# Optimization experiments

Measured on AMD Instinct MI355X. Metric: run time of the kernel, lower is better.

The kernel has to match this reference:

```python
import jax, jax.numpy as jnp
import numpy as np

MAX_ATOMS = 80
MAX_DEGREE = 4
MAX_RINGS = 10
RING_SIZE = 8
BATCH = 16384


def setup_inputs() -> dict:
    key = jax.random.key(0)
    k1, k2 = jax.random.split(key)
    # neighbor indices in [-1, MAX_ATOMS); -1 == null neighbor slot
    edges = jax.random.randint(k1, (BATCH, MAX_ATOMS, MAX_DEGREE), -1, MAX_ATOMS).astype(jnp.float32)
    # ring member atom indices in [-1, MAX_ATOMS); -1 == padding
    rings = jax.random.randint(k2, (BATCH, MAX_RINGS, RING_SIZE), -1, MAX_ATOMS).astype(jnp.int32)
    return {"edges": edges, "rings": rings}


def reference(edges, rings):
    # edges: [B, A, D] float (cast to int, -1 = null); rings: [B, R, S] int
    e = edges.astype(jnp.int32)
    B, A, D = e.shape
    R = rings.shape[1]
    # membership[b, r, a] = atom a appears in ring r of molecule b  -> [B, R, A]
    membership = jnp.any(rings[:, :, :, None] == jnp.arange(A, dtype=jnp.int32), axis=2)
    # gather neighbor membership: nbr_mem[b, r, a, d] = membership[b, r, e[b, a, d]]
    e_clip = jnp.clip(e, 0, A - 1)  # safe index for null (-1) slots, masked below
    idx = jnp.broadcast_to(e_clip.reshape(B, 1, A * D), (B, R, A * D))
    nbr_mem = jnp.take_along_axis(membership, idx, axis=2).reshape(B, R, A, D)
    # bond (a, d) is a ring bond iff some ring contains both a and its neighbor,
    # and the neighbor slot is not null
    in_ring = jnp.any(membership[:, :, :, None] & nbr_mem, axis=1)  # [B, A, D]
    valid = e != -1
    out = (in_ring & valid).astype(jnp.float32)
    return out.reshape(B, A, D, 1)
```

## Files before the change

kernel.cpp:

```cpp
#include <hip/hip_runtime.h>

#define MAX_ATOMS   80
#define MAX_DEGREE  4
#define MAX_RINGS   10
#define RING_SIZE   8
#define RING_FLAT   (MAX_RINGS * RING_SIZE)
#define EDGE_FLAT   (MAX_ATOMS * MAX_DEGREE)
#define MOLS_PER_BLOCK 4

__device__ __forceinline__ float bond_val(int nb, unsigned ma, const unsigned* m) {
    int c = nb < 0 ? 0 : (nb > MAX_ATOMS - 1 ? MAX_ATOMS - 1 : nb);
    unsigned hit = (nb >= 0) ? (ma & m[c]) : 0u;
    return hit ? 1.0f : 0.0f;
}

__global__ __launch_bounds__(256) void Find_Ring_Bonds_kernel(
    const float* __restrict__ edges,
    const int*   __restrict__ rings,
    float*       __restrict__ out,
    int B)
{
    __shared__ unsigned mask[MOLS_PER_BLOCK][MAX_ATOMS];

    const int wave = threadIdx.x >> 6;
    const int lane = threadIdx.x & 63;
    const int mol  = blockIdx.x * MOLS_PER_BLOCK + wave;
    const bool live = (mol < B);

    unsigned* m = mask[wave];

    if (live) {
        m[lane] = 0u;
        if (lane < MAX_ATOMS - 64) m[64 + lane] = 0u;
    }
    __syncthreads();

    if (live) {
        const int* ring = rings + (size_t)mol * RING_FLAT;
        int v0 = ring[lane];
        if (v0 >= 0) atomicOr(&m[v0], 1u << (lane >> 3));
        if (lane < RING_FLAT - 64) {
            int i1 = 64 + lane;
            int v1 = ring[i1];
            if (v1 >= 0) atomicOr(&m[v1], 1u << (i1 >> 3));
        }
    }
    __syncthreads();

    if (live) {
        const float4* e4 = (const float4*)(edges + (size_t)mol * EDGE_FLAT);
        float4*       o4 = (float4*)(out + (size_t)mol * EDGE_FLAT);

        {
            int a = lane;
            float4 ev = e4[a];
            unsigned ma = m[a];
            float4 r;
            r.x = bond_val((int)ev.x, ma, m);
            r.y = bond_val((int)ev.y, ma, m);
            r.z = bond_val((int)ev.z, ma, m);
            r.w = bond_val((int)ev.w, ma, m);
            o4[a] = r;
        }
        if (lane < MAX_ATOMS - 64) {
            int a = 64 + lane;
            float4 ev = e4[a];
            unsigned ma = m[a];
            float4 r;
            r.x = bond_val((int)ev.x, ma, m);
            r.y = bond_val((int)ev.y, ma, m);
            r.z = bond_val((int)ev.z, ma, m);
            r.w = bond_val((int)ev.w, ma, m);
            o4[a] = r;
        }
    }
}

extern "C" void kernel_launch(void* const* d_in, const int* in_sizes, int n_in,
                              void* d_out, int out_size, void* d_ws, size_t ws_size,
                              hipStream_t stream) {
    const float* edges = (const float*)d_in[0];
    const int*   rings = (const int*)d_in[1];
    float*       out   = (float*)d_out;

    const int B = in_sizes[0] / EDGE_FLAT;
    const int grid = (B + MOLS_PER_BLOCK - 1) / MOLS_PER_BLOCK;

    Find_Ring_Bonds_kernel<<<grid, 256, 0, stream>>>(edges, rings, out, B);
}
```

Before: 76.60 us.

## Remap to one thread per atom with 8 molecules per block and nontemporal stores

Replaces the one-wave-per-molecule mapping, where lanes 16-63 sat idle on the second pass, with a flat mapping of one thread per atom across 8 molecules per 640-thread block. Every lane now handles exactly one ring entry and one edge float4. Output writes use nontemporal stores to avoid cache pollution, and the upper clamp on neighbor indices is dropped. The cost is larger blocks and integer divide-by-80 index math, and an out-of-range neighbor index (above 79) would now read shared memory belonging to the next molecule.

```diff
diff --git a/kernel.cpp b/kernel.cpp
--- a/kernel.cpp
+++ b/kernel.cpp
@@ -2,77 +2,54 @@
 
 #define MAX_ATOMS   80
 #define MAX_DEGREE  4
-#define MAX_RINGS   10
-#define RING_SIZE   8
-#define RING_FLAT   (MAX_RINGS * RING_SIZE)
-#define EDGE_FLAT   (MAX_ATOMS * MAX_DEGREE)
-#define MOLS_PER_BLOCK 4
+#define RING_FLAT   80
+#define EDGE_FLAT   320
+#define MPB         8
+#define THREADS     (MPB * MAX_ATOMS)
 
-__device__ __forceinline__ float bond_val(int nb, unsigned ma, const unsigned* m) {
-    int c = nb < 0 ? 0 : (nb > MAX_ATOMS - 1 ? MAX_ATOMS - 1 : nb);
-    unsigned hit = (nb >= 0) ? (ma & m[c]) : 0u;
-    return hit ? 1.0f : 0.0f;
-}
+typedef float vf4 __attribute__((ext_vector_type(4)));
 
-__global__ __launch_bounds__(256) void Find_Ring_Bonds_kernel(
+__global__ __launch_bounds__(THREADS) void Find_Ring_Bonds_kernel(
     const float* __restrict__ edges,
     const int*   __restrict__ rings,
     float*       __restrict__ out,
     int B)
 {
-    __shared__ unsigned mask[MOLS_PER_BLOCK][MAX_ATOMS];
+    __shared__ unsigned mask[MPB * MAX_ATOMS];
 
-    const int wave = threadIdx.x >> 6;
-    const int lane = threadIdx.x & 63;
-    const int mol  = blockIdx.x * MOLS_PER_BLOCK + wave;
+    const int t   = threadIdx.x;
+    const int ml  = t / MAX_ATOMS;
+    const int a   = t - ml * MAX_ATOMS;
+    const int mol = blockIdx.x * MPB + ml;
     const bool live = (mol < B);
 
-    unsigned* m = mask[wave];
+    mask[t] = 0u;
+    __syncthreads();
 
     if (live) {
-        m[lane] = 0u;
-        if (lane < MAX_ATOMS - 64) m[64 + lane] = 0u;
+        int v = rings[(size_t)mol * RING_FLAT + a];
+        if (v >= 0) atomicOr(&mask[ml * MAX_ATOMS + v], 1u << (a >> 3));
     }
     __syncthreads();
 
     if (live) {
-        const int* ring = rings + (size_t)mol * RING_FLAT;
-        int v0 = ring[lane];
-        if (v0 >= 0) atomicOr(&m[v0], 1u << (lane >> 3));
-        if (lane < RING_FLAT - 64) {
-            int i1 = 64 + lane;
-            int v1 = ring[i1];
-            if (v1 >= 0) atomicOr(&m[v1], 1u << (i1 >> 3));
-        }
-    }
-    __syncthreads();
+        const unsigned* __restrict__ m = &mask[ml * MAX_ATOMS];
+        const vf4 ev = ((const vf4*)edges)[(size_t)mol * MAX_ATOMS + a];
+        const unsigned ma = m[a];
 
-    if (live) {
-        const float4* e4 = (const float4*)(edges + (size_t)mol * EDGE_FLAT);
-        float4*       o4 = (float4*)(out + (size_t)mol * EDGE_FLAT);
+        const int nx = (int)ev.x, ny = (int)ev.y, nz = (int)ev.z, nw = (int)ev.w;
+        const unsigned hx = ma & m[nx < 0 ? 0 : nx];
+        const unsigned hy = ma & m[ny < 0 ? 0 : ny];
+        const unsigned hz = ma & m[nz < 0 ? 0 : nz];
+        const unsigned hw = ma & m[nw < 0 ? 0 : nw];
 
-        {
-            int a = lane;
-            float4 ev = e4[a];
-            unsigned ma = m[a];
-            float4 r;
-            r.x = bond_val((int)ev.x, ma, m);
-            r.y = bond_val((int)ev.y, ma, m);
-            r.z = bond_val((int)ev.z, ma, m);
-            r.w = bond_val((int)ev.w, ma, m);
-            o4[a] = r;
-        }
-        if (lane < MAX_ATOMS - 64) {
-            int a = 64 + lane;
-            float4 ev = e4[a];
-            unsigned ma = m[a];
-            float4 r;
-            r.x = bond_val((int)ev.x, ma, m);
-            r.y = bond_val((int)ev.y, ma, m);
-            r.z = bond_val((int)ev.z, ma, m);
-            r.w = bond_val((int)ev.w, ma, m);
-            o4[a] = r;
-        }
+        vf4 r;
+        r.x = (nx >= 0 && hx) ? 1.0f : 0.0f;
+        r.y = (ny >= 0 && hy) ? 1.0f : 0.0f;
+        r.z = (nz >= 0 && hz) ? 1.0f : 0.0f;
+        r.w = (nw >= 0 && hw) ? 1.0f : 0.0f;
+
+        __builtin_nontemporal_store(r, &((vf4*)out)[(size_t)mol * MAX_ATOMS + a]);
     }
 }
 
@@ -84,7 +61,7 @@
     float*       out   = (float*)d_out;
 
     const int B = in_sizes[0] / EDGE_FLAT;
-    const int grid = (B + MOLS_PER_BLOCK - 1) / MOLS_PER_BLOCK;
+    const int grid = (B + MPB - 1) / MPB;
 
-    Find_Ring_Bonds_kernel<<<grid, 256, 0, stream>>>(edges, rings, out, B);
+    Find_Ring_Bonds_kernel<<<grid, THREADS, 0, stream>>>(edges, rings, out, B);
 }
```

Result: no change. 76.67 us (+0.1%).
